# Optimization experiments

Measured on AMD Instinct MI355X. Metric: run time of the kernel, lower is better.

Reference implementation:

```python
import jax, jax.numpy as jnp
import numpy as np

THETA_BASE = 10000.0


def rope(x):
    # x: [B, S, D], D even. Interleaved-pair rotary embedding.
    B, S, D = x.shape
    pos = jnp.arange(S, dtype=jnp.float32)                       # [S]
    p = jnp.arange(D // 2, dtype=jnp.float32)                    # p-1 in the torch code
    inv_freq = 1.0 / (THETA_BASE ** (2.0 * p / D))               # [D/2]
    theta = pos[:, None] * inv_freq[None, :]                     # [S, D/2]
    sin_t, cos_t = jnp.sin(theta), jnp.cos(theta)
    x1 = x[..., 0::2]                                            # [B, S, D/2]
    x2 = x[..., 1::2]
    r1 = x1 * cos_t - x2 * sin_t
    r2 = x1 * sin_t + x2 * cos_t
    return jnp.stack((r1, r2), axis=-1).reshape(B, S, D)


def setup_inputs() -> dict:
    key = jax.random.key(0)
    k_x, k_q, k_k, k_v = jax.random.split(key, 4)
    B, S, E, DH = 4, 4096, 1024, 64
    x = jax.random.normal(k_x, (B, S, E), dtype=jnp.float32)
    # causal lower-triangular mask (mask==0 positions are disallowed)
    mask = jnp.tril(jnp.ones((S, S), dtype=jnp.int32))
    W_Q = jax.random.uniform(k_q, (E, DH), dtype=jnp.float32)
    W_K = jax.random.uniform(k_k, (E, DH), dtype=jnp.float32)
    W_V = jax.random.uniform(k_v, (E, DH), dtype=jnp.float32)
    return {"x": x, "mask": mask, "W_Q": W_Q, "W_K": W_K, "W_V": W_V}


def reference(x, mask, W_Q, W_K, W_V):
    d_h = W_Q.shape[1]
    Q = x @ W_Q                                                  # [B, S, d_h]
    K = x @ W_K
    V = x @ W_V
    Q, K = rope(Q), rope(K)
    scores = jnp.einsum('bqd,bkd->bqk', Q, K) / jnp.sqrt(jnp.float32(d_h))
    masked = jnp.where(mask == 0, -jnp.inf, scores)              # broadcast [S,S] -> [B,S,S]
    attn = jax.nn.softmax(masked, axis=-1)
    return jnp.einsum('bqk,bkd->bqd', attn, V)
```

## Files before the change

kernel.cpp:

```cpp
#include <hip/hip_runtime.h>

typedef short short8  __attribute__((ext_vector_type(8)));
typedef short short4v __attribute__((ext_vector_type(4)));
typedef float f32x4   __attribute__((ext_vector_type(4)));

#define NB 4
#define NS 4096
#define NE 1024
#define ND 64

__device__ __forceinline__ short f2bf(float f) {
    unsigned u = __builtin_bit_cast(unsigned, f);
    u = (u + 0x7FFFu + ((u >> 16) & 1u)) >> 16;
    return (short)u;
}
__device__ __forceinline__ float bf2f(short s) {
    unsigned u = ((unsigned)(unsigned short)s) << 16;
    return __builtin_bit_cast(float, u);
}

#define LDS_BAR() do {                                               \
        asm volatile("s_waitcnt lgkmcnt(0)" ::: "memory");           \
        __builtin_amdgcn_s_barrier();                                \
        __builtin_amdgcn_sched_barrier(0);                           \
    } while (0)

__global__ void prep_wt(const float* __restrict__ WQ, const float* __restrict__ WK,
                        const float* __restrict__ WV,
                        short* __restrict__ wtp_hi, short* __restrict__ wtp_lo) {
    int idx = blockIdx.x * 256 + threadIdx.x;
    if (idx >= 192 * NE) return;
    int n = idx >> 10, k = idx & (NE - 1);
    int sel = n >> 6, d = n & 63;
    const float* W = (sel == 0) ? WQ : (sel == 1 ? WK : WV);
    float v = W[k * ND + d];
    if (sel == 0) v *= 0.125f;
    short hi = f2bf(v);
    short lo = f2bf(v - bf2f(hi));
    int off = ((k >> 5) * 12 + (n >> 4)) * 512 + ((k & 31) >> 3) * 128 + (n & 15) * 8 + (k & 7);
    wtp_hi[off] = hi;
    wtp_lo[off] = lo;
}

__global__ __launch_bounds__(256, 2) void proj_rope(
        const float* __restrict__ x,
        const short* __restrict__ wtp_hi, const short* __restrict__ wtp_lo,
        short* __restrict__ qhi, short* __restrict__ qlo,
        short* __restrict__ kfph, short* __restrict__ kfpl,
        short* __restrict__ vfp) {
    __shared__ short Xh[32 * 64], Xl[32 * 64];
    __shared__ short Vlds[64 * 32];
    const int tid = threadIdx.x;
    const int w = tid >> 6, lane = tid & 63;
    const int g = lane >> 4, cl = lane & 15;
    const int rb = blockIdx.x << 5;

    f32x4 acc[2][3];
    #pragma unroll
    for (int i = 0; i < 2; ++i)
        #pragma unroll
        for (int j = 0; j < 3; ++j) acc[i][j] = (f32x4){0.f, 0.f, 0.f, 0.f};

    const int srow = tid >> 3, skc = tid & 7;
    const float* xs0 = x + (size_t)(rb + srow) * NE + (skc << 3);
    const int swoff = srow * 64 + ((skc ^ (srow & 7)) << 3);

    const short* bph = wtp_hi + (size_t)w * 512 + (lane << 3);
    const short* bpl = wtp_lo + (size_t)w * 512 + (lane << 3);

    float4 xa0, xa1, xb0, xb1;
    short8 b0[6], b1[6];

#define LOADXA(kk) { xa0 = *(const float4*)(xs0 + (kk)); \
                     xa1 = *(const float4*)(xs0 + (kk) + 4); }
#define LOADXB(kk) { xb0 = *(const float4*)(xs0 + (kk)); \
                     xb1 = *(const float4*)(xs0 + (kk) + 4); }
#define LOADB(Bs, kk) {                                                      \
        const int ko = ((kk) >> 5) * 6144;                                   \
        _Pragma("unroll")                                                    \
        for (int ct = 0; ct < 3; ++ct) {                                     \
            Bs[ct * 2] = *(const short8*)(bph + ko + ct * 2048);             \
            if (ct < 2)                                                      \
                Bs[ct * 2 + 1] = *(const short8*)(bpl + ko + ct * 2048);     \
        } }
#define CONV(X0, X1, h8, l8) {                                               \
        float vv[8] = {X0.x, X0.y, X0.z, X0.w, X1.x, X1.y, X1.z, X1.w};      \
        _Pragma("unroll")                                                    \
        for (int q = 0; q < 8; ++q) {                                        \
            short h = f2bf(vv[q]);                                           \
            h8[q] = h;                                                       \
            l8[q] = f2bf(vv[q] - bf2f(h));                                   \
        } }
#define HALF(h, Bs) {                                                        \
        _Pragma("unroll")                                                    \
        for (int rt = 0; rt < 2; ++rt) {                                     \
            const int R = (rt << 4) + cl;                                    \
            const int ro = R * 64 + ((((h) * 4 + g) ^ (R & 7)) << 3);        \
            short8 ah = *(const short8*)(Xh + ro);                           \
            short8 al = *(const short8*)(Xl + ro);                           \
            _Pragma("unroll")                                                \
            for (int ct = 0; ct < 2; ++ct) {                                 \
                acc[rt][ct] = __builtin_amdgcn_mfma_f32_16x16x32_bf16(ah, Bs[ct*2],   acc[rt][ct], 0, 0, 0); \
                acc[rt][ct] = __builtin_amdgcn_mfma_f32_16x16x32_bf16(ah, Bs[ct*2+1], acc[rt][ct], 0, 0, 0); \
                acc[rt][ct] = __builtin_amdgcn_mfma_f32_16x16x32_bf16(al, Bs[ct*2],   acc[rt][ct], 0, 0, 0); \
            }                                                                \
            acc[rt][2] = __builtin_amdgcn_mfma_f32_16x16x32_bf16(ah, Bs[4], acc[rt][2], 0, 0, 0); \
        } }

    LOADXA(0); LOADXB(64);
    LOADB(b0, 0);

    #pragma unroll 1
    for (int k0 = 0; k0 < NE; k0 += 128) {
        {
            short8 h8, l8;
            CONV(xa0, xa1, h8, l8);
            LDS_BAR();
            *(short8*)(Xh + swoff) = h8;
            *(short8*)(Xl + swoff) = l8;
            if (k0 + 128 < NE) LOADXA(k0 + 128);
            LOADB(b1, k0 + 32);
            LDS_BAR();
            HALF(0, b0);
            LOADB(b0, k0 + 64);
            HALF(1, b1);
        }
        {
            short8 h8, l8;
            CONV(xb0, xb1, h8, l8);
            LDS_BAR();
            *(short8*)(Xh + swoff) = h8;
            *(short8*)(Xl + swoff) = l8;
            if (k0 + 192 < NE) LOADXB(k0 + 192);
            LOADB(b1, k0 + 96);
            LDS_BAR();
            HALF(0, b0);
            if (k0 + 128 < NE) LOADB(b0, k0 + 128);
            HALF(1, b1);
        }
    }
#undef LOADXA
#undef LOADXB
#undef LOADB
#undef CONV
#undef HALF

    __syncthreads();

    #pragma unroll
    for (int rt = 0; rt < 2; ++rt) {
        #pragma unroll
        for (int ct = 0; ct < 3; ++ct) {
            int c = ((w + (ct << 2)) << 4) + cl;
            #pragma unroll
            for (int r = 0; r < 4; ++r) {
                int row = rb + (rt << 4) + (g << 2) + r;
                int sl = row & 31;
                float val = acc[rt][ct][r];
                if (c < 128) {
                    int d = c & 63;
                    int p = d >> 1;
                    float freq = exp2f(-(float)p * 0.41524101186091903f);
                    float theta = (float)(row & (NS - 1)) * freq;
                    float sn = sinf(theta), cs = cosf(theta);
                    float partner = __shfl_xor(val, 1);
                    float rot = (c & 1) ? fmaf(partner, sn, val * cs)
                                        : fmaf(-partner, sn, val * cs);
                    short hi = f2bf(rot);
                    short lo = f2bf(rot - bf2f(hi));
                    if (c < 64) {
                        int off = row * ND + d;
                        qhi[off] = hi; qlo[off] = lo;
                    } else {
                        Xh[sl * 64 + d] = hi;
                        Xl[sl * 64 + d] = lo;
                    }
                } else {
                    Vlds[(c - 128) * 32 + sl] = f2bf(val);
                }
            }
        }
    }
    __syncthreads();

    {
        const size_t tbase = ((size_t)((rb >> 12) << 7) + ((rb & (NS - 1)) >> 5)) * 2048;
        {
            const int ci = (tid >> 7) & 1, hf = (tid >> 6) & 1, ln = tid & 63;
            const int src = (ci * 16 + (ln & 15)) * 64 + hf * 32 + (ln >> 4) * 8;
            *(short8*)(kfph + tbase + tid * 8) = *(const short8*)(Xh + src);
            *(short8*)(kfpl + tbase + tid * 8) = *(const short8*)(Xl + src);
        }
        if (tid < 256) {
            const int dt = (tid >> 6) & 3, ln = tid & 63;
            const int src = (dt * 16 + (ln & 15)) * 32 + (ln >> 4) * 8;
            *(short8*)(vfp + tbase + tid * 8) = *(const short8*)(Vlds + src);
        }
    }
}

__global__ __launch_bounds__(256, 4) void attn_fused(
        const short* __restrict__ qhi, const short* __restrict__ qlo,
        const short* __restrict__ kfph, const short* __restrict__ kfpl,
        const short* __restrict__ vfp, float* __restrict__ outp) {
    __shared__ short Ps[4][16][40];
    __shared__ float Co[4][16][66];
    __shared__ float Cm[4][16], Cls[4][16];
    const int tid = threadIdx.x;
    const int lane = tid & 63, w = tid >> 6;
    const int g = lane >> 4, cl = lane & 15;
    const int bid = blockIdx.x;
    const int b = (bid >> 1) & 3;
    const int t = 255 - (((bid >> 3) << 1) | (bid & 1));
    const int qw = t << 4;
    const int rowb = b << 12;

    short8 qh[2], ql[2];
    #pragma unroll
    for (int ks = 0; ks < 2; ++ks) {
        int off = ((rowb + qw + cl) << 6) + (ks << 5) + (g << 3);
        qh[ks] = *(const short8*)(qhi + off);
        ql[ks] = *(const short8*)(qlo + off);
    }

    f32x4 o[4];
    #pragma unroll
    for (int i = 0; i < 4; ++i) o[i] = (f32x4){0.f, 0.f, 0.f, 0.f};
    float m = -1e38f, lsp = 0.f;

    const int nkv = (t >> 1) + 1;
    const short* kbaseh = kfph + (size_t)(b << 7) * 2048 + (lane << 3);
    const short* kbasel = kfpl + (size_t)(b << 7) * 2048 + (lane << 3);
    const short* vbase  = vfp  + (size_t)(b << 7) * 2048 + (lane << 3);

    short8 kf[2][4];
    short8 vf[4];

#define LOADK(jj) {                                                          \
        _Pragma("unroll")                                                    \
        for (int ci = 0; ci < 2; ++ci) {                                     \
            const short* kh = kbaseh + (jj) * 2048 + ci * 1024;              \
            const short* kl = kbasel + (jj) * 2048 + ci * 1024;              \
            kf[ci][0] = *(const short8*)(kh);                                \
            kf[ci][1] = *(const short8*)(kh + 512);                          \
            kf[ci][2] = *(const short8*)(kl);                                \
            kf[ci][3] = *(const short8*)(kl + 512);                          \
        } }
#define LOADV(jj) {                                                          \
        _Pragma("unroll")                                                    \
        for (int dt = 0; dt < 4; ++dt)                                       \
            vf[dt] = *(const short8*)(vbase + (jj) * 2048 + dt * 512);       \
        }

    if (w < nkv) {
        LOADK(w); LOADV(w);
        #pragma unroll 1
        for (int j = w; j < nkv; j += 4) {
            f32x4 sc[2];
            #pragma unroll
            for (int ci = 0; ci < 2; ++ci) {
                f32x4 s = (f32x4){0.f, 0.f, 0.f, 0.f};
                s = __builtin_amdgcn_mfma_f32_16x16x32_bf16(kf[ci][0], qh[0], s, 0, 0, 0);
                s = __builtin_amdgcn_mfma_f32_16x16x32_bf16(kf[ci][1], qh[1], s, 0, 0, 0);
                s = __builtin_amdgcn_mfma_f32_16x16x32_bf16(kf[ci][0], ql[0], s, 0, 0, 0);
                s = __builtin_amdgcn_mfma_f32_16x16x32_bf16(kf[ci][1], ql[1], s, 0, 0, 0);
                s = __builtin_amdgcn_mfma_f32_16x16x32_bf16(kf[ci][2], qh[0], s, 0, 0, 0);
                s = __builtin_amdgcn_mfma_f32_16x16x32_bf16(kf[ci][3], qh[1], s, 0, 0, 0);
                sc[ci] = s;
            }
            const int jn = j + 4;
            if (jn < nkv) LOADK(jn);

            if (j == nkv - 1) {
                #pragma unroll
                for (int ci = 0; ci < 2; ++ci)
                    #pragma unroll
                    for (int r = 0; r < 4; ++r)
                        if ((j << 5) + (ci << 4) + (g << 2) + r > qw + cl) sc[ci][r] = -1e30f;
            }
            float pm = fmaxf(fmaxf(fmaxf(sc[0][0], sc[0][1]), fmaxf(sc[0][2], sc[0][3])),
                             fmaxf(fmaxf(sc[1][0], sc[1][1]), fmaxf(sc[1][2], sc[1][3])));
            pm = fmaxf(pm, __shfl_xor(pm, 16));
            pm = fmaxf(pm, __shfl_xor(pm, 32));
            const float mo = m;
            m = fmaxf(m, pm);
            const float rs = __expf(mo - m);
            float psum = 0.f;
            #pragma unroll
            for (int ci = 0; ci < 2; ++ci) {
                float p0 = __expf(sc[ci][0] - m), p1 = __expf(sc[ci][1] - m);
                float p2 = __expf(sc[ci][2] - m), p3 = __expf(sc[ci][3] - m);
                psum += (p0 + p1) + (p2 + p3);
                short4v pk;
                pk[0] = f2bf(p0); pk[1] = f2bf(p1); pk[2] = f2bf(p2); pk[3] = f2bf(p3);
                *(short4v*)(&Ps[w][cl][(ci << 4) + (g << 2)]) = pk;
            }
            lsp = lsp * rs + psum;
            if (__any(m > mo)) {
                float rs4[4];
                #pragma unroll
                for (int r = 0; r < 4; ++r) rs4[r] = __shfl(rs, (g << 2) + r);
                #pragma unroll
                for (int dt = 0; dt < 4; ++dt)
                    #pragma unroll
                    for (int r = 0; r < 4; ++r) o[dt][r] *= rs4[r];
            }
            short8 pa = *(short8*)(&Ps[w][cl][g << 3]);
            #pragma unroll
            for (int dt = 0; dt < 4; ++dt)
                o[dt] = __builtin_amdgcn_mfma_f32_16x16x32_bf16(pa, vf[dt], o[dt], 0, 0, 0);
            if (jn < nkv) LOADV(jn);
        }
    }
#undef LOADK
#undef LOADV

    lsp += __shfl_xor(lsp, 16);
    lsp += __shfl_xor(lsp, 32);
    if (g == 0) { Cm[w][cl] = m; Cls[w][cl] = lsp; }
    #pragma unroll
    for (int dt = 0; dt < 4; ++dt)
        #pragma unroll
        for (int r = 0; r < 4; ++r)
            Co[w][(g << 2) + r][(dt << 4) + cl] = o[dt][r];
    __syncthreads();

    if (w == 0) {
        #pragma unroll
        for (int r = 0; r < 4; ++r) {
            const int row = (g << 2) + r;
            float M = fmaxf(fmaxf(Cm[0][row], Cm[1][row]), fmaxf(Cm[2][row], Cm[3][row]));
            float e0 = __expf(Cm[0][row] - M), e1 = __expf(Cm[1][row] - M);
            float e2 = __expf(Cm[2][row] - M), e3 = __expf(Cm[3][row] - M);
            float L = Cls[0][row] * e0 + Cls[1][row] * e1 + Cls[2][row] * e2 + Cls[3][row] * e3;
            float inv = 1.f / L;
            #pragma unroll
            for (int dt = 0; dt < 4; ++dt) {
                int d = (dt << 4) + cl;
                float O = Co[0][row][d] * e0 + Co[1][row][d] * e1
                        + Co[2][row][d] * e2 + Co[3][row][d] * e3;
                outp[(rowb + qw + row) * ND + d] = O * inv;
            }
        }
    }
}

extern "C" void kernel_launch(void* const* d_in, const int* in_sizes, int n_in,
                              void* d_out, int out_size, void* d_ws, size_t ws_size,
                              hipStream_t stream) {
    const float* x  = (const float*)d_in[0];
    const float* WQ = (const float*)d_in[2];
    const float* WK = (const float*)d_in[3];
    const float* WV = (const float*)d_in[4];

    const size_t need = 786432u + 5u * 2097152u;
    if (ws_size < need) return;

    char* ws = (char*)d_ws;
    short* wtph = (short*)(ws);
    short* wtpl = (short*)(ws + 393216);
    short* qhi  = (short*)(ws + 786432);
    short* qlo  = (short*)(ws + 786432 + 1 * 2097152);
    short* kfph = (short*)(ws + 786432 + 2 * 2097152);
    short* kfpl = (short*)(ws + 786432 + 3 * 2097152);
    short* vfp  = (short*)(ws + 786432 + 4 * 2097152);

    prep_wt<<<768, 256, 0, stream>>>(WQ, WK, WV, wtph, wtpl);
    proj_rope<<<512, 256, 0, stream>>>(x, wtph, wtpl, qhi, qlo, kfph, kfpl, vfp);
    attn_fused<<<1024, 256, 0, stream>>>(qhi, qlo, kfph, kfpl, vfp, (float*)d_out);
}
```

Before: 72.79 us.

## Split projection GEMM along K into two partial kernels plus combine

Splits the QKV projection's 1024-long reduction into two halves, running 1024 blocks that each write fp32 partial accumulators to workspace, then a combine kernel that sums the partials and applies RoPE and the packed stores. The aim is more blocks in flight to fill the GPU's compute units, since the projection previously launched only 512 blocks. In exchange it adds an extra launch and about 12 MB of partial-sum global traffic. If the workspace is too small it falls back to the original fused kernel.

Result: slower. 79.17 us (+8.8%).

```diff
diff --git a/kernel.cpp b/kernel.cpp
--- a/kernel.cpp
+++ b/kernel.cpp
@@ -42,18 +42,60 @@
     wtp_lo[off] = lo;
 }
 
-__global__ __launch_bounds__(256, 2) void proj_rope(
+#define PROJ_LOOP_BODY(KB, KE)                                               \
+    LOADXA(KB); LOADXB((KB) + 64);                                           \
+    LOADB(b0, KB);                                                           \
+    _Pragma("unroll 1")                                                      \
+    for (int k0 = (KB); k0 < (KE); k0 += 128) {                              \
+        {                                                                    \
+            short8 h8, l8;                                                   \
+            CONV(xa0, xa1, h8, l8);                                          \
+            LDS_BAR();                                                       \
+            *(short8*)(Xh + swoff) = h8;                                     \
+            *(short8*)(Xl + swoff) = l8;                                     \
+            if (k0 + 128 < (KE)) LOADXA(k0 + 128);                           \
+            LOADB(b1, k0 + 32);                                              \
+            LDS_BAR();                                                       \
+            HALF(0, b0);                                                     \
+            LOADB(b0, k0 + 64);                                              \
+            HALF(1, b1);                                                     \
+        }                                                                    \
+        {                                                                    \
+            short8 h8, l8;                                                   \
+            CONV(xb0, xb1, h8, l8);                                          \
+            LDS_BAR();                                                       \
+            *(short8*)(Xh + swoff) = h8;                                     \
+            *(short8*)(Xl + swoff) = l8;                                     \
+            if (k0 + 192 < (KE)) LOADXB(k0 + 192);                           \
+            LOADB(b1, k0 + 96);                                              \
+            LDS_BAR();                                                       \
+            HALF(0, b0);                                                     \
+            if (k0 + 128 < (KE)) LOADB(b0, k0 + 128);                        \
+            HALF(1, b1);                                                     \
+        }                                                                    \
+    }
+
+#define PROJ_MACROS                                                          \
+_Pragma("push_macro(\"X\")")
+
+#define DECL_LOOP_MACROS                                                     \
+    float4 xa0, xa1, xb0, xb1;                                               \
+    short8 b0[6], b1[6];
+
+#define DEF_LOADX                                                            \
+
+__global__ __launch_bounds__(256, 2) void proj_partial(
         const float* __restrict__ x,
         const short* __restrict__ wtp_hi, const short* __restrict__ wtp_lo,
-        short* __restrict__ qhi, short* __restrict__ qlo,
-        short* __restrict__ kfph, short* __restrict__ kfpl,
-        short* __restrict__ vfp) {
+        f32x4* __restrict__ pacc) {
     __shared__ short Xh[32 * 64], Xl[32 * 64];
-    __shared__ short Vlds[64 * 32];
     const int tid = threadIdx.x;
     const int w = tid >> 6, lane = tid & 63;
     const int g = lane >> 4, cl = lane & 15;
-    const int rb = blockIdx.x << 5;
+    const int bid = blockIdx.x;
+    const int ks = bid >> 9, tile = bid & 511;
+    const int rb = tile << 5;
+    const int kb = ks << 9, ke = kb + 512;
 
     f32x4 acc[2][3];
     #pragma unroll
@@ -107,45 +149,45 @@
             acc[rt][2] = __builtin_amdgcn_mfma_f32_16x16x32_bf16(ah, Bs[4], acc[rt][2], 0, 0, 0); \
         } }
 
-    LOADXA(0); LOADXB(64);
-    LOADB(b0, 0);
-
-    #pragma unroll 1
-    for (int k0 = 0; k0 < NE; k0 += 128) {
-        {
-            short8 h8, l8;
-            CONV(xa0, xa1, h8, l8);
-            LDS_BAR();
-            *(short8*)(Xh + swoff) = h8;
-            *(short8*)(Xl + swoff) = l8;
-            if (k0 + 128 < NE) LOADXA(k0 + 128);
-            LOADB(b1, k0 + 32);
-            LDS_BAR();
-            HALF(0, b0);
-            LOADB(b0, k0 + 64);
-            HALF(1, b1);
-        }
-        {
-            short8 h8, l8;
-            CONV(xb0, xb1, h8, l8);
-            LDS_BAR();
-            *(short8*)(Xh + swoff) = h8;
-            *(short8*)(Xl + swoff) = l8;
-            if (k0 + 192 < NE) LOADXB(k0 + 192);
-            LOADB(b1, k0 + 96);
-            LDS_BAR();
-            HALF(0, b0);
-            if (k0 + 128 < NE) LOADB(b0, k0 + 128);
-            HALF(1, b1);
-        }
-    }
+    PROJ_LOOP_BODY(kb, ke)
 #undef LOADXA
 #undef LOADXB
 #undef LOADB
 #undef CONV
 #undef HALF
 
-    __syncthreads();
+    f32x4* base = pacc + ((size_t)bid * 6) * 256 + tid;
+    #pragma unroll
+    for (int rt = 0; rt < 2; ++rt)
+        #pragma unroll
+        for (int ct = 0; ct < 3; ++ct)
+            base[(rt * 3 + ct) * 256] = acc[rt][ct];
+}
+
+__global__ __launch_bounds__(256) void proj_combine(
+        const f32x4* __restrict__ pacc,
+        short* __restrict__ qhi, short* __restrict__ qlo,
+        short* __restrict__ kfph, short* __restrict__ kfpl,
+        short* __restrict__ vfp) {
+    __shared__ short Xh[32 * 64], Xl[32 * 64];
+    __shared__ short Vlds[64 * 32];
+    const int tid = threadIdx.x;
+    const int w = tid >> 6, lane = tid & 63;
+    const int g = lane >> 4, cl = lane & 15;
+    const int tile = blockIdx.x;
+    const int rb = tile << 5;
+
+    f32x4 acc[2][3];
+    const f32x4* p0 = pacc + ((size_t)tile * 6) * 256 + tid;
+    const f32x4* p1 = pacc + ((size_t)(tile + 512) * 6) * 256 + tid;
+    #pragma unroll
+    for (int rt = 0; rt < 2; ++rt)
+        #pragma unroll
+        for (int ct = 0; ct < 3; ++ct) {
+            f32x4 a = p0[(rt * 3 + ct) * 256];
+            f32x4 b = p1[(rt * 3 + ct) * 256];
+            acc[rt][ct] = a + b;
+        }
 
     #pragma unroll
     for (int rt = 0; rt < 2; ++rt) {
@@ -199,6 +241,130 @@
     }
 }
 
+__global__ __launch_bounds__(256, 2) void proj_rope_full(
+        const float* __restrict__ x,
+        const short* __restrict__ wtp_hi, const short* __restrict__ wtp_lo,
+        short* __restrict__ qhi, short* __restrict__ qlo,
+        short* __restrict__ kfph, short* __restrict__ kfpl,
+        short* __restrict__ vfp) {
+    __shared__ short Xh[32 * 64], Xl[32 * 64];
+    __shared__ short Vlds[64 * 32];
+    const int tid = threadIdx.x;
+    const int w = tid >> 6, lane = tid & 63;
+    const int g = lane >> 4, cl = lane & 15;
+    const int rb = blockIdx.x << 5;
+
+    f32x4 acc[2][3];
+    #pragma unroll
+    for (int i = 0; i < 2; ++i)
+        #pragma unroll
+        for (int j = 0; j < 3; ++j) acc[i][j] = (f32x4){0.f, 0.f, 0.f, 0.f};
+
+    const int srow = tid >> 3, skc = tid & 7;
+    const float* xs0 = x + (size_t)(rb + srow) * NE + (skc << 3);
+    const int swoff = srow * 64 + ((skc ^ (srow & 7)) << 3);
+
+    const short* bph = wtp_hi + (size_t)w * 512 + (lane << 3);
+    const short* bpl = wtp_lo + (size_t)w * 512 + (lane << 3);
+
+    float4 xa0, xa1, xb0, xb1;
+    short8 b0[6], b1[6];
+
+#define LOADXA(kk) { xa0 = *(const float4*)(xs0 + (kk)); \
+                     xa1 = *(const float4*)(xs0 + (kk) + 4); }
+#define LOADXB(kk) { xb0 = *(const float4*)(xs0 + (kk)); \
+                     xb1 = *(const float4*)(xs0 + (kk) + 4); }
+#define LOADB(Bs, kk) {                                                      \
+        const int ko = ((kk) >> 5) * 6144;                                   \
+        _Pragma("unroll")                                                    \
+        for (int ct = 0; ct < 3; ++ct) {                                     \
+            Bs[ct * 2] = *(const short8*)(bph + ko + ct * 2048);             \
+            if (ct < 2)                                                      \
+                Bs[ct * 2 + 1] = *(const short8*)(bpl + ko + ct * 2048);     \
+        } }
+#define CONV(X0, X1, h8, l8) {                                               \
+        float vv[8] = {X0.x, X0.y, X0.z, X0.w, X1.x, X1.y, X1.z, X1.w};      \
+        _Pragma("unroll")                                                    \
+        for (int q = 0; q < 8; ++q) {                                        \
+            short h = f2bf(vv[q]);                                           \
+            h8[q] = h;                                                       \
+            l8[q] = f2bf(vv[q] - bf2f(h));                                   \
+        } }
+#define HALF(h, Bs) {                                                        \
+        _Pragma("unroll")                                                    \
+        for (int rt = 0; rt < 2; ++rt) {                                     \
+            const int R = (rt << 4) + cl;                                    \
+            const int ro = R * 64 + ((((h) * 4 + g) ^ (R & 7)) << 3);        \
+            short8 ah = *(const short8*)(Xh + ro);                           \
+            short8 al = *(const short8*)(Xl + ro);                           \
+            _Pragma("unroll")                                                \
+            for (int ct = 0; ct < 2; ++ct) {                                 \
+                acc[rt][ct] = __builtin_amdgcn_mfma_f32_16x16x32_bf16(ah, Bs[ct*2],   acc[rt][ct], 0, 0, 0); \
+                acc[rt][ct] = __builtin_amdgcn_mfma_f32_16x16x32_bf16(ah, Bs[ct*2+1], acc[rt][ct], 0, 0, 0); \
+                acc[rt][ct] = __builtin_amdgcn_mfma_f32_16x16x32_bf16(al, Bs[ct*2],   acc[rt][ct], 0, 0, 0); \
+            }                                                                \
+            acc[rt][2] = __builtin_amdgcn_mfma_f32_16x16x32_bf16(ah, Bs[4], acc[rt][2], 0, 0, 0); \
+        } }
+
+    PROJ_LOOP_BODY(0, NE)
+#undef LOADXA
+#undef LOADXB
+#undef LOADB
+#undef CONV
+#undef HALF
+
+    __syncthreads();
+    #pragma unroll
+    for (int rt = 0; rt < 2; ++rt) {
+        #pragma unroll
+        for (int ct = 0; ct < 3; ++ct) {
+            int c = ((w + (ct << 2)) << 4) + cl;
+            #pragma unroll
+            for (int r = 0; r < 4; ++r) {
+                int row = rb + (rt << 4) + (g << 2) + r;
+                int sl = row & 31;
+                float val = acc[rt][ct][r];
+                if (c < 128) {
+                    int d = c & 63;
+                    int p = d >> 1;
+                    float freq = exp2f(-(float)p * 0.41524101186091903f);
+                    float theta = (float)(row & (NS - 1)) * freq;
+                    float sn = sinf(theta), cs = cosf(theta);
+                    float partner = __shfl_xor(val, 1);
+                    float rot = (c & 1) ? fmaf(partner, sn, val * cs)
+                                        : fmaf(-partner, sn, val * cs);
+                    short hi = f2bf(rot);
+                    short lo = f2bf(rot - bf2f(hi));
+                    if (c < 64) {
+                        int off = row * ND + d;
+                        qhi[off] = hi; qlo[off] = lo;
+                    } else {
+                        Xh[sl * 64 + d] = hi;
+                        Xl[sl * 64 + d] = lo;
+                    }
+                } else {
+                    Vlds[(c - 128) * 32 + sl] = f2bf(val);
+                }
+            }
+        }
+    }
+    __syncthreads();
+    {
+        const size_t tbase = ((size_t)((rb >> 12) << 7) + ((rb & (NS - 1)) >> 5)) * 2048;
+        {
+            const int ci = (tid >> 7) & 1, hf = (tid >> 6) & 1, ln = tid & 63;
+            const int src = (ci * 16 + (ln & 15)) * 64 + hf * 32 + (ln >> 4) * 8;
+            *(short8*)(kfph + tbase + tid * 8) = *(const short8*)(Xh + src);
+            *(short8*)(kfpl + tbase + tid * 8) = *(const short8*)(Xl + src);
+        }
+        if (tid < 256) {
+            const int dt = (tid >> 6) & 3, ln = tid & 63;
+            const int src = (dt * 16 + (ln & 15)) * 32 + (ln >> 4) * 8;
+            *(short8*)(vfp + tbase + tid * 8) = *(const short8*)(Vlds + src);
+        }
+    }
+}
+
 __global__ __launch_bounds__(256, 4) void attn_fused(
         const short* __restrict__ qhi, const short* __restrict__ qlo,
         const short* __restrict__ kfph, const short* __restrict__ kfpl,
@@ -353,8 +519,10 @@
     const float* WK = (const float*)d_in[3];
     const float* WV = (const float*)d_in[4];
 
-    const size_t need = 786432u + 5u * 2097152u;
-    if (ws_size < need) return;
+    const size_t need_base = 786432u + 5u * 2097152u;
+    const size_t pacc_sz   = 2u * 512u * 6u * 256u * 16u;
+    const size_t need_split = need_base + pacc_sz;
+    if (ws_size < need_base) return;
 
     char* ws = (char*)d_ws;
     short* wtph = (short*)(ws);
@@ -364,8 +532,14 @@
     short* kfph = (short*)(ws + 786432 + 2 * 2097152);
     short* kfpl = (short*)(ws + 786432 + 3 * 2097152);
     short* vfp  = (short*)(ws + 786432 + 4 * 2097152);
+    f32x4* pacc = (f32x4*)(ws + need_base);
 
     prep_wt<<<768, 256, 0, stream>>>(WQ, WK, WV, wtph, wtpl);
-    proj_rope<<<512, 256, 0, stream>>>(x, wtph, wtpl, qhi, qlo, kfph, kfpl, vfp);
+    if (ws_size >= need_split) {
+        proj_partial<<<1024, 256, 0, stream>>>(x, wtph, wtpl, pacc);
+        proj_combine<<<512, 256, 0, stream>>>(pacc, qhi, qlo, kfph, kfpl, vfp);
+    } else {
+        proj_rope_full<<<512, 256, 0, stream>>>(x, wtph, wtpl, qhi, qlo, kfph, kfpl, vfp);
+    }
     attn_fused<<<1024, 256, 0, stream>>>(qhi, qlo, kfph, kfpl, vfp, (float*)d_out);
 }
```
